# Kernel tuning notes

Hardware: AMD Instinct MI355X
Metric: run time of the kernel (lower is better)

Reference implementation:

```python
import jax, jax.numpy as jnp
import numpy as np

D, H, L, E, K, FF, VIS, NC, NT = 1024, 8, 4, 4, 2, 2048, 1536, 4, 4
HD = D // H


def layer_norm(x, g, b, eps=1e-5):
    m = x.mean(-1, keepdims=True)
    v = ((x - m) ** 2).mean(-1, keepdims=True)
    return (x - m) / jnp.sqrt(v + eps) * g + b


def sinusoidal_pos(seq_len):
    pos = jnp.arange(seq_len, dtype=jnp.float32)[:, None]
    div = jnp.exp(jnp.arange(0, D, 2, dtype=jnp.float32) * (-jnp.log(10000.0) / D))
    pe = jnp.zeros((seq_len, D), dtype=jnp.float32)
    pe = pe.at[:, 0::2].set(jnp.sin(pos * div))
    pe = pe.at[:, 1::2].set(jnp.cos(pos * div))
    return pe


def mha(x, wi, bi, wo, bo):
    # wi: [D, 3D] (pre-transposed), wo: [D, D]
    B, S, _ = x.shape
    qkv = x @ wi + bi
    q, k, v = jnp.split(qkv, 3, axis=-1)
    split = lambda t: t.reshape(B, S, H, HD).transpose(0, 2, 1, 3)
    q, k, v = split(q), split(k), split(v)
    scores = jnp.einsum('bhqd,bhkd->bhqk', q, k) / jnp.sqrt(jnp.float32(HD))
    a = jax.nn.softmax(scores, axis=-1)
    o = jnp.einsum('bhqk,bhkd->bhqd', a, v).transpose(0, 2, 1, 3).reshape(B, S, D)
    return o @ wo + bo


def moe(x_flat, rw, rb, w1, b1, w2, b2):
    # x_flat: [N, D]; rw: [D, E]; w1: [E, D, FF]; w2: [E, FF, D]
    logits = x_flat @ rw + rb                      # [N, E]
    topv, topi = jax.lax.top_k(logits, K)          # [N, K]
    probs = jax.nn.softmax(topv, axis=-1)          # softmax over the top-k logits
    onehot = jax.nn.one_hot(topi, E, dtype=x_flat.dtype)      # [N, K, E]
    combine = jnp.einsum('nk,nke->ne', probs, onehot)         # [N, E]
    h = jax.nn.relu(jnp.einsum('nd,edf->enf', x_flat, w1) + b1[:, None, :])  # [E, N, FF]
    o = jnp.einsum('enf,efd->end', h, w2) + b2[:, None, :]                   # [E, N, D]
    return jnp.einsum('ne,end->nd', combine, o)


def setup_inputs() -> dict:
    key = jax.random.key(0)
    ks = iter(jax.random.split(key, 32))
    s = 0.02
    n = lambda shape: jax.random.normal(next(ks), shape, dtype=jnp.float32) * s
    inp = {
        'vis_feat': jax.random.normal(next(ks), (64, 128, VIS), dtype=jnp.float32),
        'proj_w': n((VIS, D)), 'proj_b': jnp.zeros((D,), jnp.float32),
        'in_proj_w': n((L, D, 3 * D)), 'in_proj_b': jnp.zeros((L, 3 * D), jnp.float32),
        'out_proj_w': n((L, D, D)), 'out_proj_b': jnp.zeros((L, D), jnp.float32),
        'ln1_g': jnp.ones((L, D), jnp.float32), 'ln1_b': jnp.zeros((L, D), jnp.float32),
        'ln2_g': jnp.ones((L, D), jnp.float32), 'ln2_b': jnp.zeros((L, D), jnp.float32),
        'router_w': n((L, D, E)), 'router_b': jnp.zeros((L, E), jnp.float32),
        'ew1': n((L, E, D, FF)), 'eb1': jnp.zeros((L, E, FF), jnp.float32),
        'ew2': n((L, E, FF, D)), 'eb2': jnp.zeros((L, E, D), jnp.float32),
        'attn_w': n((D, 1)), 'attn_b': jnp.zeros((1,), jnp.float32),
        'heads_w': n((NT, D, NC)), 'heads_b': jnp.zeros((NT, NC), jnp.float32),
    }
    return inp


def reference(vis_feat, proj_w, proj_b, in_proj_w, in_proj_b, out_proj_w, out_proj_b,
              ln1_g, ln1_b, ln2_g, ln2_b, router_w, router_b, ew1, eb1, ew2, eb2,
              attn_w, attn_b, heads_w, heads_b):
    B, S, _ = vis_feat.shape
    x = vis_feat @ proj_w + proj_b            # projection to d_model=1024
    x = x + sinusoidal_pos(S)[None]           # positional encoding
    for l in range(L):                         # 4 MoE transformer layers
        x = layer_norm(x + mha(x, in_proj_w[l], in_proj_b[l], out_proj_w[l], out_proj_b[l]),
                       ln1_g[l], ln1_b[l])
        moe_out = moe(x.reshape(B * S, D), router_w[l], router_b[l],
                      ew1[l], eb1[l], ew2[l], eb2[l]).reshape(B, S, D)
        x = layer_norm(x + moe_out, ln2_g[l], ln2_b[l])
    # attention pooling over time, then 4 task heads
    scores = jax.nn.softmax(x @ attn_w + attn_b, axis=1)   # [B, S, 1]
    pooled = jnp.sum(scores * x, axis=1)                   # [B, D]
    logits = jnp.einsum('bd,tdc->tbc', pooled, heads_w) + heads_b[:, None, :]  # [4, B, 4]
    return logits
```

## Files before the change

### kernel.cpp

```cpp
#include <hip/hip_runtime.h>
#include <hip/hip_bf16.h>

typedef unsigned short u16;
typedef unsigned int u32;
using short8 = __attribute__((ext_vector_type(8))) short;
using f32x4  = __attribute__((ext_vector_type(4))) float;

__device__ __forceinline__ u16 f2bu(float f) {
  u32 u = __builtin_bit_cast(u32, f);
  u32 r = u + 0x7fffu + ((u >> 16) & 1u);
  return (u16)(r >> 16);
}
__device__ __forceinline__ float bu2f(u16 u) {
  u32 x = ((u32)u) << 16;
  return __builtin_bit_cast(float, x);
}
__device__ __forceinline__ float waveRedSum(float v) {
  #pragma unroll
  for (int off = 32; off > 0; off >>= 1) v += __shfl_xor(v, off, 64);
  return v;
}
__device__ __forceinline__ void gload16(const void* g, void* l) {
  __builtin_amdgcn_global_load_lds((const __attribute__((address_space(1))) u32*)g,
                                   (__attribute__((address_space(3))) u32*)l, 16, 0, 0);
}

template<int MODE>
__global__ __launch_bounds__(256) void gemm_bt(
    const u16* __restrict__ A, const u16* __restrict__ Bt, const float* __restrict__ bias,
    float* __restrict__ Cf, u16* __restrict__ Cb, u16* __restrict__ M0, u16* __restrict__ M1,
    const int* __restrict__ tok, const float* __restrict__ prob, const int* __restrict__ slot,
    const int* __restrict__ poff, const int* __restrict__ cnts,
    int N, int K)
{
  const int gx = gridDim.x;
  const int nwg = gx * gridDim.y;
  int lid = blockIdx.y * gx + blockIdx.x;
  lid = (lid & 7) * (nwg >> 3) + (lid >> 3);
  const int brow = (lid / gx) << 7, bcol = (lid % gx) << 7;

  int e = 0, rowEnd = 0;
  const u16* Bw = Bt;
  const float* bw = bias;
  if constexpr (MODE >= 2) {
    if (brow >= poff[4]) return;
    #pragma unroll
    for (int q = 1; q < 4; ++q) if (brow >= poff[q]) e = q;
    rowEnd = poff[e] + cnts[e];
    Bw = Bt + (size_t)e * N * K;
    bw = bias + e * N;
  }

  __shared__ __align__(16) u16 As[128 * 32];
  __shared__ __align__(16) u16 Bs[128 * 32];
  const int tid = threadIdx.x;
  const int wave = tid >> 6, lane = tid & 63;
  const int wr = wave >> 1, wc = wave & 1;
  const int r = lane & 15, kg = lane >> 4;

  f32x4 acc[4][4];
  #pragma unroll
  for (int m = 0; m < 4; ++m)
    #pragma unroll
    for (int n = 0; n < 4; ++n) acc[m][n] = f32x4{0.f, 0.f, 0.f, 0.f};

  const int c0 = (wave << 6) + lane;
  const int row0 = c0 >> 2, col0 = (c0 & 3) << 3;
  const int c1 = 256 + c0;
  const int row1 = c1 >> 2, col1 = (c1 & 3) << 3;

  size_t ar0, ar1;
  if constexpr (MODE == 2) {
    const int g0 = brow + row0, g1 = brow + row1;
    ar0 = (size_t)tok[(g0 < rowEnd) ? g0 : poff[e]];
    ar1 = (size_t)tok[(g1 < rowEnd) ? g1 : poff[e]];
  } else {
    ar0 = (size_t)(brow + row0);
    ar1 = (size_t)(brow + row1);
  }
  const u16* Bb = Bw + (size_t)bcol * K;

  for (int k0 = 0; k0 < K; k0 += 32) {
    __syncthreads();
    gload16(A + ar0 * K + k0 + col0, &As[(wave << 6) * 8]);
    gload16(Bb + (size_t)row0 * K + k0 + col0, &Bs[(wave << 6) * 8]);
    gload16(A + ar1 * K + k0 + col1, &As[(256 + (wave << 6)) * 8]);
    gload16(Bb + (size_t)row1 * K + k0 + col1, &Bs[(256 + (wave << 6)) * 8]);
    __syncthreads();
    short8 a[4], b[4];
    #pragma unroll
    for (int m = 0; m < 4; ++m)
      a[m] = *(const short8*)&As[((wr << 6) + (m << 4) + r) * 32 + (kg << 3)];
    #pragma unroll
    for (int n = 0; n < 4; ++n)
      b[n] = *(const short8*)&Bs[((wc << 6) + (n << 4) + r) * 32 + (kg << 3)];
    #pragma unroll
    for (int m = 0; m < 4; ++m)
      #pragma unroll
      for (int n = 0; n < 4; ++n)
        acc[m][n] = __builtin_amdgcn_mfma_f32_16x16x32_bf16(a[m], b[n], acc[m][n], 0, 0, 0);
  }

  if constexpr (MODE == 3) {
    #pragma unroll
    for (int m = 0; m < 4; ++m) {
      #pragma unroll
      for (int i4 = 0; i4 < 4; ++i4) {
        const int row = brow + (wr << 6) + (m << 4) + (kg << 2) + i4;
        if (row < rowEnd) {
          const int t = tok[row];
          const float pp = prob[row];
          u16* dst = slot[row] ? M1 : M0;
          #pragma unroll
          for (int n = 0; n < 4; ++n) {
            const int col = bcol + (wc << 6) + (n << 4) + r;
            dst[(size_t)t * N + col] = f2bu((acc[m][n][i4] + bw[col]) * pp);
          }
        }
      }
    }
  } else {
    #pragma unroll
    for (int m = 0; m < 4; ++m) {
      #pragma unroll
      for (int n = 0; n < 4; ++n) {
        const int col = bcol + (wc << 6) + (n << 4) + r;
        const float bv = bw[col];
        #pragma unroll
        for (int i4 = 0; i4 < 4; ++i4) {
          const int row = brow + (wr << 6) + (m << 4) + (kg << 2) + i4;
          const float v = acc[m][n][i4] + bv;
          const size_t off = (size_t)row * N + col;
          if constexpr (MODE == 0) Cf[off] = v;
          else if constexpr (MODE == 1) Cb[off] = f2bu(v);
          else Cb[off] = f2bu(fmaxf(v, 0.f));
        }
      }
    }
  }
}

__device__ __forceinline__ void tconv_tile(const float* __restrict__ s, u16* __restrict__ d,
                                           int K, int N, int n0, int k0)
{
  __shared__ float t[32][33];
  const int x = threadIdx.x, y = threadIdx.y;
  #pragma unroll
  for (int j = 0; j < 4; ++j) t[y + 8 * j][x] = s[(size_t)(k0 + y + 8 * j) * N + n0 + x];
  __syncthreads();
  #pragma unroll
  for (int j = 0; j < 4; ++j) d[(size_t)(n0 + y + 8 * j) * K + k0 + x] = f2bu(t[x][y + 8 * j]);
}

__global__ __launch_bounds__(256) void tconv_kernel(const float* __restrict__ src, u16* __restrict__ dst,
                                                    int K, int N)
{
  tconv_tile(src, dst, K, N, blockIdx.x << 5, blockIdx.y << 5);
}

__global__ __launch_bounds__(256) void tconv4_kernel(
    const float* __restrict__ wqkv_s, const float* __restrict__ wout_s,
    const float* __restrict__ we1_s, const float* __restrict__ we2_s,
    u16* __restrict__ wqkv_d, u16* __restrict__ wout_d,
    u16* __restrict__ we1_d, u16* __restrict__ we2_d)
{
  const int bid = blockIdx.x;
  if (bid < 3072) {
    tconv_tile(wqkv_s, wqkv_d, 1024, 3072, (bid % 96) << 5, (bid / 96) << 5);
  } else if (bid < 4096) {
    const int b2 = bid - 3072;
    tconv_tile(wout_s, wout_d, 1024, 1024, (b2 % 32) << 5, (b2 / 32) << 5);
  } else if (bid < 12288) {
    const int b2 = bid - 4096;
    const int ee = b2 >> 11, rr = b2 & 2047;
    tconv_tile(we1_s + (size_t)ee * 2048 * 1024, we1_d + (size_t)ee * 2048 * 1024,
               1024, 2048, (rr % 64) << 5, (rr / 64) << 5);
  } else {
    const int b2 = bid - 12288;
    const int ee = b2 >> 11, rr = b2 & 2047;
    tconv_tile(we2_s + (size_t)ee * 1024 * 2048, we2_d + (size_t)ee * 1024 * 2048,
               2048, 1024, (rr % 32) << 5, (rr / 32) << 5);
  }
}

__global__ __launch_bounds__(256) void conv_kernel(const float* __restrict__ in, u16* __restrict__ out)
{
  const size_t i = ((size_t)blockIdx.x * 256 + threadIdx.x) * 4;
  float4 v = *(const float4*)(in + i);
  *(ushort4*)(out + i) = make_ushort4(f2bu(v.x), f2bu(v.y), f2bu(v.z), f2bu(v.w));
}

__global__ __launch_bounds__(256) void pe_kernel(float* __restrict__ X, u16* __restrict__ Xb)
{
  const int idx = blockIdx.x * 256 + threadIdx.x;
  const int d = idx & 1023;
  const int s = (idx >> 10) & 127;
  const float de = (float)(d & ~1);
  const float ang = (float)s * expf(de * (-9.210340371976184f / 1024.f));
  const float pe = (d & 1) ? cosf(ang) : sinf(ang);
  const float v = X[idx] + pe;
  X[idx] = v;
  Xb[idx] = f2bu(v);
}

__global__ __launch_bounds__(256) void ln_kernel(const float* __restrict__ Xi, const u16* __restrict__ R,
    const float* __restrict__ g, const float* __restrict__ be,
    const float* __restrict__ rw, const float* __restrict__ rb,
    float* __restrict__ Xo, u16* __restrict__ Xbo,
    int* __restrict__ choice, float* __restrict__ prob2)
{
  const int token = blockIdx.x;
  const size_t base = (size_t)token << 10;
  const int tid = threadIdx.x;
  float vals[4]; float s = 0.f, s2 = 0.f;
  #pragma unroll
  for (int j = 0; j < 4; ++j) {
    const int d = tid + (j << 8);
    const float v = Xi[base + d] + bu2f(R[base + d]);
    vals[j] = v; s += v; s2 += v * v;
  }
  s = waveRedSum(s); s2 = waveRedSum(s2);
  __shared__ float rs[4], rs2[4];
  __shared__ float rl[4][4];
  const int wave = tid >> 6, lane = tid & 63;
  if (lane == 0) { rs[wave] = s; rs2[wave] = s2; }
  __syncthreads();
  s = rs[0] + rs[1] + rs[2] + rs[3];
  s2 = rs2[0] + rs2[1] + rs2[2] + rs2[3];
  const float mean = s * (1.f / 1024.f);
  const float var = s2 * (1.f / 1024.f) - mean * mean;
  const float inv = rsqrtf(var + 1e-5f);
  float l0 = 0.f, l1 = 0.f, l2 = 0.f, l3 = 0.f;
  #pragma unroll
  for (int j = 0; j < 4; ++j) {
    const int d = tid + (j << 8);
    const float y = (vals[j] - mean) * inv * g[d] + be[d];
    Xo[base + d] = y;
    Xbo[base + d] = f2bu(y);
    const float4 w = *(const float4*)(rw + ((size_t)d << 2));
    l0 += y * w.x; l1 += y * w.y; l2 += y * w.z; l3 += y * w.w;
  }
  l0 = waveRedSum(l0); l1 = waveRedSum(l1); l2 = waveRedSum(l2); l3 = waveRedSum(l3);
  if (lane == 0) { rl[wave][0] = l0; rl[wave][1] = l1; rl[wave][2] = l2; rl[wave][3] = l3; }
  __syncthreads();
  if (tid == 0) {
    float v[4];
    #pragma unroll
    for (int q = 0; q < 4; ++q)
      v[q] = rl[0][q] + rl[1][q] + rl[2][q] + rl[3][q] + rb[q];
    int i1 = 0;
    for (int q = 1; q < 4; ++q) if (v[q] > v[i1]) i1 = q;
    int i2 = (i1 == 0) ? 1 : 0;
    for (int q = 0; q < 4; ++q) if (q != i1 && v[q] > v[i2]) i2 = q;
    const float p2 = __expf(v[i2] - v[i1]);
    const float is = 1.f / (1.f + p2);
    choice[token] = i1 | (i2 << 8);
    prob2[token * 2]     = is;
    prob2[token * 2 + 1] = p2 * is;
  }
}

__global__ __launch_bounds__(256) void ln2_kernel(const float* __restrict__ Xi,
    const u16* __restrict__ R0, const u16* __restrict__ R1,
    const float* __restrict__ g, const float* __restrict__ be,
    float* __restrict__ Xo, u16* __restrict__ Xbo,
    const float* __restrict__ aw, const float* __restrict__ ab, float* __restrict__ S)
{
  const int token = blockIdx.x;
  const size_t base = (size_t)token << 10;
  const int tid = threadIdx.x;
  float vals[4]; float s = 0.f, s2 = 0.f;
  #pragma unroll
  for (int j = 0; j < 4; ++j) {
    const int d = tid + (j << 8);
    const float v = Xi[base + d] + (bu2f(R0[base + d]) + bu2f(R1[base + d]));
    vals[j] = v; s += v; s2 += v * v;
  }
  s = waveRedSum(s); s2 = waveRedSum(s2);
  __shared__ float rs[4], rs2[4];
  __shared__ float rsc[4];
  const int wave = tid >> 6, lane = tid & 63;
  if (lane == 0) { rs[wave] = s; rs2[wave] = s2; }
  __syncthreads();
  s = rs[0] + rs[1] + rs[2] + rs[3];
  s2 = rs2[0] + rs2[1] + rs2[2] + rs2[3];
  const float mean = s * (1.f / 1024.f);
  const float var = s2 * (1.f / 1024.f) - mean * mean;
  const float inv = rsqrtf(var + 1e-5f);
  float sc = 0.f;
  #pragma unroll
  for (int j = 0; j < 4; ++j) {
    const int d = tid + (j << 8);
    const float y = (vals[j] - mean) * inv * g[d] + be[d];
    Xo[base + d] = y;
    Xbo[base + d] = f2bu(y);
    if (aw) sc += y * aw[d];
  }
  if (aw) {
    sc = waveRedSum(sc);
    if (lane == 0) rsc[wave] = sc;
    __syncthreads();
    if (tid == 0) S[token] = rsc[0] + rsc[1] + rsc[2] + rsc[3] + ab[0];
  }
}

#define LDW 136
__global__ __launch_bounds__(256) void attn_mfma_kernel(const u16* __restrict__ QKVb, u16* __restrict__ ATTb)
{
  __shared__ __align__(16) u16 Kb[128 * LDW];
  __shared__ __align__(16) u16 Vt[128 * LDW];
  u16* Pb = Kb;
  const int b = blockIdx.x >> 3, h = blockIdx.x & 7;
  const int tid = threadIdx.x;
  const int wave = tid >> 6, lane = tid & 63;
  const int r = lane & 15, kg = lane >> 4;
  const u16* base = QKVb + (size_t)b * 128 * 3072 + h * 128;

  for (int i = tid; i < 128 * 16; i += 256) {
    const int row = i >> 4, c8 = (i & 15) << 3;
    *(short8*)&Kb[row * LDW + c8] = *(const short8*)(base + (size_t)row * 3072 + 1024 + c8);
  }
  for (int i = tid; i < 128 * 128; i += 256) {
    const int d = i & 127, key = i >> 7;
    Vt[d * LDW + key] = base[(size_t)key * 3072 + 2048 + d];
  }

  short8 a[2][4];
  #pragma unroll
  for (int m = 0; m < 2; ++m) {
    const int row = wave * 32 + m * 16 + r;
    const u16* qp = base + (size_t)row * 3072;
    #pragma unroll
    for (int ks = 0; ks < 4; ++ks)
      a[m][ks] = *(const short8*)(qp + ks * 32 + kg * 8);
  }
  __syncthreads();

  f32x4 acc[2][8];
  #pragma unroll
  for (int m = 0; m < 2; ++m)
    #pragma unroll
    for (int n = 0; n < 8; ++n) acc[m][n] = f32x4{0.f, 0.f, 0.f, 0.f};
  #pragma unroll
  for (int n = 0; n < 8; ++n) {
    #pragma unroll
    for (int ks = 0; ks < 4; ++ks) {
      short8 bf = *(const short8*)&Kb[(n * 16 + r) * LDW + ks * 32 + kg * 8];
      #pragma unroll
      for (int m = 0; m < 2; ++m)
        acc[m][n] = __builtin_amdgcn_mfma_f32_16x16x32_bf16(a[m][ks], bf, acc[m][n], 0, 0, 0);
    }
  }
  __syncthreads();

  const float sc = 0.08838834764831845f;
  #pragma unroll
  for (int m = 0; m < 2; ++m) {
    #pragma unroll
    for (int i = 0; i < 4; ++i) {
      float mx = -1e30f;
      #pragma unroll
      for (int n = 0; n < 8; ++n) mx = fmaxf(mx, acc[m][n][i]);
      #pragma unroll
      for (int msk = 1; msk < 16; msk <<= 1) mx = fmaxf(mx, __shfl_xor(mx, msk, 64));
      float s = 0.f;
      #pragma unroll
      for (int n = 0; n < 8; ++n) { float pv = __expf((acc[m][n][i] - mx) * sc); acc[m][n][i] = pv; s += pv; }
      #pragma unroll
      for (int msk = 1; msk < 16; msk <<= 1) s += __shfl_xor(s, msk, 64);
      const float inv = 1.f / s;
      #pragma unroll
      for (int n = 0; n < 8; ++n) {
        const int prow = wave * 32 + m * 16 + kg * 4 + i;
        Pb[prow * LDW + n * 16 + r] = f2bu(acc[m][n][i] * inv);
      }
    }
  }

  f32x4 oacc[2][8];
  #pragma unroll
  for (int m = 0; m < 2; ++m)
    #pragma unroll
    for (int n = 0; n < 8; ++n) oacc[m][n] = f32x4{0.f, 0.f, 0.f, 0.f};
  #pragma unroll
  for (int ks = 0; ks < 4; ++ks) {
    short8 pa[2];
    #pragma unroll
    for (int m = 0; m < 2; ++m)
      pa[m] = *(const short8*)&Pb[(wave * 32 + m * 16 + r) * LDW + ks * 32 + kg * 8];
    #pragma unroll
    for (int n = 0; n < 8; ++n) {
      short8 vb = *(const short8*)&Vt[(n * 16 + r) * LDW + ks * 32 + kg * 8];
      #pragma unroll
      for (int m = 0; m < 2; ++m)
        oacc[m][n] = __builtin_amdgcn_mfma_f32_16x16x32_bf16(pa[m], vb, oacc[m][n], 0, 0, 0);
    }
  }

  u16* op = ATTb + ((size_t)b * 128) * 1024 + h * 128;
  #pragma unroll
  for (int m = 0; m < 2; ++m) {
    #pragma unroll
    for (int n = 0; n < 8; ++n) {
      #pragma unroll
      for (int i = 0; i < 4; ++i) {
        const int row = wave * 32 + m * 16 + kg * 4 + i;
        op[(size_t)row * 1024 + n * 16 + r] = f2bu(oacc[m][n][i]);
      }
    }
  }
}
#undef LDW

__global__ __launch_bounds__(256) void build_lists_kernel(
    const int* __restrict__ choice, const float* __restrict__ prob2,
    int* __restrict__ cnt, int* __restrict__ poff,
    int* __restrict__ tok, float* __restrict__ prob, int* __restrict__ slot)
{
  const int tid = threadIdx.x;
  const int e = tid >> 6, lane = tid & 63;
  const int t0 = lane << 7;
  int mycount = 0;
  for (int j = 0; j < 128; ++j) {
    const int c = choice[t0 + j];
    mycount += (((c & 255) == e) || ((c >> 8) == e)) ? 1 : 0;
  }
  int incl = mycount;
  #pragma unroll
  for (int off = 1; off < 64; off <<= 1) {
    const int t = __shfl_up(incl, off, 64);
    if (lane >= off) incl += t;
  }
  __shared__ int totals[4];
  if (lane == 63) totals[e] = incl;
  __syncthreads();
  int base = 0;
  #pragma unroll
  for (int q = 0; q < 4; ++q)
    if (q < e) base += (totals[q] + 255) & ~255;
  int pos = base + incl - mycount;
  for (int j = 0; j < 128; ++j) {
    const int token = t0 + j;
    const int c = choice[token];
    const int m = ((c & 255) == e) ? 1 : (((c >> 8) == e) ? 2 : 0);
    if (m) {
      tok[pos] = token;
      prob[pos] = prob2[token * 2 + (m - 1)];
      slot[pos] = m - 1;
      ++pos;
    }
  }
  if (lane == 0) {
    cnt[e] = totals[e];
    poff[e] = base;
    if (e == 3) poff[4] = base + ((totals[3] + 255) & ~255);
  }
}

__global__ __launch_bounds__(256) void pool_kernel(const float* __restrict__ X, const float* __restrict__ S,
                                                   float* __restrict__ P)
{
  const int b = blockIdx.x;
  const int tid = threadIdx.x;
  __shared__ float p[128];
  if (tid < 128) p[tid] = S[b * 128 + tid];
  __syncthreads();
  float mx = -1e30f;
  for (int t = 0; t < 128; ++t) mx = fmaxf(mx, p[t]);
  float sum = 0.f;
  for (int t = 0; t < 128; ++t) sum += __expf(p[t] - mx);
  const float inv = 1.f / sum;
  __syncthreads();
  if (tid < 128) p[tid] = __expf(p[tid] - mx) * inv;
  __syncthreads();
  float acc[4] = {0.f, 0.f, 0.f, 0.f};
  for (int t = 0; t < 128; ++t) {
    const float pt = p[t];
    const float* xp = X + ((size_t)(b * 128 + t) << 10) + tid;
    #pragma unroll
    for (int j = 0; j < 4; ++j) acc[j] += pt * xp[j << 8];
  }
  #pragma unroll
  for (int j = 0; j < 4; ++j) P[((size_t)b << 10) + tid + (j << 8)] = acc[j];
}

__global__ __launch_bounds__(256) void heads_kernel(const float* __restrict__ P, const float* __restrict__ hw,
    const float* __restrict__ hb, float* __restrict__ out)
{
  const int idx = blockIdx.x * 4 + (threadIdx.x >> 6);
  const int lane = threadIdx.x & 63;
  const int t = idx >> 8, b = (idx >> 2) & 63, c = idx & 3;
  const float* pp = P + ((size_t)b << 10);
  const float* wp = hw + (size_t)t * 4096 + c;
  float s = 0.f;
  #pragma unroll
  for (int j = 0; j < 16; ++j) { const int k = lane + (j << 6); s += pp[k] * wp[(size_t)k << 2]; }
  s = waveRedSum(s);
  if (lane == 0) out[idx] = s + hb[t * 4 + c];
}

extern "C" void kernel_launch(void* const* d_in, const int* in_sizes, int n_in,
                              void* d_out, int out_size, void* d_ws, size_t ws_size,
                              hipStream_t stream)
{
  (void)in_sizes; (void)n_in; (void)out_size; (void)ws_size;
  const float* vis        = (const float*)d_in[0];
  const float* proj_w     = (const float*)d_in[1];
  const float* proj_b     = (const float*)d_in[2];
  const float* in_proj_w  = (const float*)d_in[3];
  const float* in_proj_b  = (const float*)d_in[4];
  const float* out_proj_w = (const float*)d_in[5];
  const float* out_proj_b = (const float*)d_in[6];
  const float* ln1_g      = (const float*)d_in[7];
  const float* ln1_b      = (const float*)d_in[8];
  const float* ln2_g      = (const float*)d_in[9];
  const float* ln2_b      = (const float*)d_in[10];
  const float* router_w   = (const float*)d_in[11];
  const float* router_b   = (const float*)d_in[12];
  const float* ew1        = (const float*)d_in[13];
  const float* eb1        = (const float*)d_in[14];
  const float* ew2        = (const float*)d_in[15];
  const float* eb2        = (const float*)d_in[16];
  const float* attn_w     = (const float*)d_in[17];
  const float* attn_b     = (const float*)d_in[18];
  const float* heads_w    = (const float*)d_in[19];
  const float* heads_b    = (const float*)d_in[20];
  float* out = (float*)d_out;

  char* p = (char*)d_ws;
  auto take = [&](size_t bytes) -> char* {
    char* q = p; p += (bytes + 255) & ~(size_t)255; return q;
  };
  float* X    = (float*)take(8192ULL * 1024 * 4);
  u16*   Xb   = (u16*)  take(8192ULL * 1024 * 2);
  char*  QKVr = take(104857600ULL);
  u16*   ATTb = (u16*)  take(8192ULL * 1024 * 2);
  int*   CNT  = (int*)  take(4 * 4);
  int*   POFF = (int*)  take(5 * 4);
  int*   CHOICE = (int*)take(8192ULL * 4);
  float* PROB2  = (float*)take(8192ULL * 2 * 4);
  int*   TOK  = (int*)  take(17408ULL * 4);
  float* PROB = (float*)take(17408ULL * 4);
  int*   SLOT = (int*)  take(17408ULL * 4);
  float* S    = (float*)take(8192ULL * 4);
  float* POOL = (float*)take(64ULL * 1024 * 4);
  u16*   Wqkv = (u16*)  take(3072ULL * 1024 * 2);
  u16*   Wout = (u16*)  take(1024ULL * 1024 * 2);
  u16*   We1  = (u16*)  take(4ULL * 2048 * 1024 * 2);
  u16*   We2  = (u16*)  take(4ULL * 1024 * 2048 * 2);
  u16*   QKVb  = (u16*)QKVr;
  u16*   O16   = (u16*)QKVr;
  u16*   H     = (u16*)QKVr;
  u16*   MOE0b = (u16*)(QKVr + 71303168);
  u16*   MOE1b = (u16*)(QKVr + 71303168 + 16777216);
  u16*   Wproj = We1;
  u16*   VISb  = (u16*)QKVr;

  const dim3 tb(32, 8);
  #define GARGS Cf_, Cb_, MOE0b, MOE1b, TOK, PROB, SLOT, POFF, CNT

  tconv_kernel<<<dim3(1024 / 32, 1536 / 32), tb, 0, stream>>>(proj_w, Wproj, 1536, 1024);
  conv_kernel<<<(8192 * 1536 / 4) / 256, 256, 0, stream>>>(vis, VISb);
  {
    float* Cf_ = X; u16* Cb_ = nullptr;
    gemm_bt<0><<<dim3(8, 64), 256, 0, stream>>>(VISb, Wproj, proj_b, GARGS, 1024, 1536);
  }
  pe_kernel<<<8192 * 1024 / 256, 256, 0, stream>>>(X, Xb);

  for (int l = 0; l < 4; ++l) {
    tconv4_kernel<<<20480, tb, 0, stream>>>(
        in_proj_w + (size_t)l * 1024 * 3072, out_proj_w + (size_t)l * 1024 * 1024,
        ew1 + (size_t)l * 4 * 1024 * 2048, ew2 + (size_t)l * 4 * 2048 * 1024,
        Wqkv, Wout, We1, We2);

    {
      float* Cf_ = nullptr; u16* Cb_ = QKVb;
      gemm_bt<1><<<dim3(24, 64), 256, 0, stream>>>(Xb, Wqkv, in_proj_b + l * 3072, GARGS, 3072, 1024);
    }
    attn_mfma_kernel<<<512, 256, 0, stream>>>(QKVb, ATTb);
    {
      float* Cf_ = nullptr; u16* Cb_ = O16;
      gemm_bt<1><<<dim3(8, 64), 256, 0, stream>>>(ATTb, Wout, out_proj_b + l * 1024, GARGS, 1024, 1024);
    }
    ln_kernel<<<8192, 256, 0, stream>>>(X, O16, ln1_g + l * 1024, ln1_b + l * 1024,
                                        router_w + (size_t)l * 4096, router_b + l * 4,
                                        X, Xb, CHOICE, PROB2);
    build_lists_kernel<<<1, 256, 0, stream>>>(CHOICE, PROB2, CNT, POFF, TOK, PROB, SLOT);
    {
      float* Cf_ = nullptr; u16* Cb_ = H;
      gemm_bt<2><<<dim3(16, 136), 256, 0, stream>>>(Xb, We1, eb1 + (size_t)l * 4 * 2048, GARGS, 2048, 1024);
    }
    {
      float* Cf_ = nullptr; u16* Cb_ = nullptr;
      gemm_bt<3><<<dim3(8, 136), 256, 0, stream>>>(H, We2, eb2 + (size_t)l * 4 * 1024, GARGS, 1024, 2048);
    }
    ln2_kernel<<<8192, 256, 0, stream>>>(X, MOE0b, MOE1b, ln2_g + l * 1024, ln2_b + l * 1024,
                                         X, Xb, (l == 3) ? attn_w : nullptr, attn_b, S);
  }

  pool_kernel<<<64, 256, 0, stream>>>(X, S, POOL);
  heads_kernel<<<256, 256, 0, stream>>>(POOL, heads_w, heads_b, out);
  #undef GARGS
}
```

Before: 1.962 ms.

## Replace 128x128 GEMM with 256x256 double-buffered swizzled 8-wave kernel

Swaps the single-buffered 128x128x32 bf16 GEMM for a 512-thread kernel computing 256x256 tiles with a K step of 64. Tiles are staged through double-buffered, XOR-swizzled LDS using direct global-to-LDS loads. The main loop interleaves the prefetch loads with four MFMA quarters, separated by explicit sched barriers, waitcnt and setprio. The aim is more data reuse per loaded byte, fewer LDS bank conflicts, and overlap of global loads with matrix math. The trade-offs are lower occupancy (one large block per CU, 128 KB of LDS) and 256-row tiles in the MoE grouped GEMMs, which assumes the expert row offsets line up with the larger tile.

```diff
diff --git a/kernel.cpp b/kernel.cpp
--- a/kernel.cpp
+++ b/kernel.cpp
@@ -25,8 +25,12 @@
                                    (__attribute__((address_space(3))) u32*)l, 16, 0, 0);
 }
 
+#define SB() __builtin_amdgcn_sched_barrier(0)
+#define BARR() do { SB(); __builtin_amdgcn_s_barrier(); SB(); } while (0)
+#define VMC2() do { SB(); asm volatile("s_waitcnt vmcnt(2)" ::: "memory"); SB(); } while (0)
+
 template<int MODE>
-__global__ __launch_bounds__(256) void gemm_bt(
+__global__ __launch_bounds__(512, 1) void gemm8(
     const u16* __restrict__ A, const u16* __restrict__ Bt, const float* __restrict__ bias,
     float* __restrict__ Cf, u16* __restrict__ Cb, u16* __restrict__ M0, u16* __restrict__ M1,
     const int* __restrict__ tok, const float* __restrict__ prob, const int* __restrict__ slot,
@@ -37,7 +41,7 @@
   const int nwg = gx * gridDim.y;
   int lid = blockIdx.y * gx + blockIdx.x;
   lid = (lid & 7) * (nwg >> 3) + (lid >> 3);
-  const int brow = (lid / gx) << 7, bcol = (lid % gx) << 7;
+  const int brow = (lid / gx) << 8, bcol = (lid % gx) << 8;
 
   int e = 0, rowEnd = 0;
   const u16* Bw = Bt;
@@ -51,62 +55,98 @@
     bw = bias + e * N;
   }
 
-  __shared__ __align__(16) u16 As[128 * 32];
-  __shared__ __align__(16) u16 Bs[128 * 32];
+  __shared__ __align__(16) u16 As[32768];
+  __shared__ __align__(16) u16 Bs[32768];
+
   const int tid = threadIdx.x;
   const int wave = tid >> 6, lane = tid & 63;
-  const int wr = wave >> 1, wc = wave & 1;
+  const int wr = wave >> 2, wc = wave & 3;
   const int r = lane & 15, kg = lane >> 4;
 
-  f32x4 acc[4][4];
-  #pragma unroll
-  for (int m = 0; m < 4; ++m)
+  const int srow = tid >> 3;
+  const int sc8 = (tid & 7) ^ (srow & 7);
+
+  int tokA[2][2];
+  if constexpr (MODE == 2) {
+    #pragma unroll
+    for (int h = 0; h < 2; ++h)
+      #pragma unroll
+      for (int j = 0; j < 2; ++j) {
+        const int g = brow + h * 128 + srow + j * 64;
+        tokA[h][j] = tok[(g < rowEnd) ? g : poff[e]];
+      }
+  }
+
+#define STA(c, kt, h) do { \
+  _Pragma("unroll") for (int j_ = 0; j_ < 2; ++j_) { \
+    size_t gr_; \
+    if constexpr (MODE == 2) gr_ = (size_t)tokA[h][j_]; \
+    else gr_ = (size_t)(brow + (h) * 128 + srow + j_ * 64); \
+    gload16(A + gr_ * K + ((kt) << 6) + (sc8 << 3), \
+            &As[((c) << 14) + ((h) << 13) + (j_ << 12) + (tid << 3)]); \
+  } } while (0)
+
+#define STB(c, kt, h) do { \
+  _Pragma("unroll") for (int j_ = 0; j_ < 2; ++j_) { \
+    const size_t gr_ = (size_t)(bcol + (h) * 128 + srow + j_ * 64); \
+    gload16(Bw + gr_ * K + ((kt) << 6) + (sc8 << 3), \
+            &Bs[((c) << 14) + ((h) << 13) + (j_ << 12) + (tid << 3)]); \
+  } } while (0)
+
+  short8 afr[4], bfr[4];
+  f32x4 acc[8][4];
+  #pragma unroll
+  for (int m = 0; m < 8; ++m)
     #pragma unroll
     for (int n = 0; n < 4; ++n) acc[m][n] = f32x4{0.f, 0.f, 0.f, 0.f};
 
-  const int c0 = (wave << 6) + lane;
-  const int row0 = c0 >> 2, col0 = (c0 & 3) << 3;
-  const int c1 = 256 + c0;
-  const int row1 = c1 >> 2, col1 = (c1 & 3) << 3;
-
-  size_t ar0, ar1;
-  if constexpr (MODE == 2) {
-    const int g0 = brow + row0, g1 = brow + row1;
-    ar0 = (size_t)tok[(g0 < rowEnd) ? g0 : poff[e]];
-    ar1 = (size_t)tok[(g1 < rowEnd) ? g1 : poff[e]];
-  } else {
-    ar0 = (size_t)(brow + row0);
-    ar1 = (size_t)(brow + row1);
-  }
-  const u16* Bb = Bw + (size_t)bcol * K;
-
-  for (int k0 = 0; k0 < K; k0 += 32) {
-    __syncthreads();
-    gload16(A + ar0 * K + k0 + col0, &As[(wave << 6) * 8]);
-    gload16(Bb + (size_t)row0 * K + k0 + col0, &Bs[(wave << 6) * 8]);
-    gload16(A + ar1 * K + k0 + col1, &As[(256 + (wave << 6)) * 8]);
-    gload16(Bb + (size_t)row1 * K + k0 + col1, &Bs[(256 + (wave << 6)) * 8]);
-    __syncthreads();
-    short8 a[4], b[4];
-    #pragma unroll
-    for (int m = 0; m < 4; ++m)
-      a[m] = *(const short8*)&As[((wr << 6) + (m << 4) + r) * 32 + (kg << 3)];
-    #pragma unroll
-    for (int n = 0; n < 4; ++n)
-      b[n] = *(const short8*)&Bs[((wc << 6) + (n << 4) + r) * 32 + (kg << 3)];
-    #pragma unroll
-    for (int m = 0; m < 4; ++m)
-      #pragma unroll
-      for (int n = 0; n < 4; ++n)
-        acc[m][n] = __builtin_amdgcn_mfma_f32_16x16x32_bf16(a[m], b[n], acc[m][n], 0, 0, 0);
+#define LDA(c, MQ, KS) { _Pragma("unroll") for (int mm = 0; mm < 4; ++mm) { \
+    const int Rl = (MQ) * 64 + mm * 16 + r; \
+    const int c8 = (KS) * 4 + kg; \
+    afr[mm] = *(const short8*)&As[((c) << 14) + (wr << 13) + Rl * 64 + ((c8 ^ (Rl & 7)) << 3)]; } }
+#define LDB(c, KS) { _Pragma("unroll") for (int nn = 0; nn < 4; ++nn) { \
+    const int colL = wc * 64 + nn * 16 + r; \
+    const int c8 = (KS) * 4 + kg; \
+    const int Rl = colL & 127; \
+    bfr[nn] = *(const short8*)&Bs[((c) << 14) + ((colL >> 7) << 13) + Rl * 64 + ((c8 ^ (Rl & 7)) << 3)]; } }
+#define MFMAQ(MQ) do { __builtin_amdgcn_s_setprio(1); \
+  _Pragma("unroll") for (int nn = 0; nn < 4; ++nn) \
+  _Pragma("unroll") for (int mm = 0; mm < 4; ++mm) \
+    acc[(MQ) * 4 + mm][nn] = __builtin_amdgcn_mfma_f32_16x16x32_bf16(afr[mm], bfr[nn], acc[(MQ) * 4 + mm][nn], 0, 0, 0); \
+  __builtin_amdgcn_s_setprio(0); } while (0)
+
+  const int NT = K >> 6;
+  STB(0, 0, 0); STB(0, 0, 1); STA(0, 0, 0); STA(0, 0, 1);
+  STB(1, 1, 0);
+  VMC2();
+  BARR();
+
+  for (int t = 0; t < NT; ++t) {
+    const int cb = t & 1, nb = cb ^ 1;
+    int t1 = t + 1; if (t1 >= NT) t1 -= NT;
+    int t2 = t + 2; if (t2 >= NT) t2 -= NT;
+    LDA(cb, 0, 0); LDB(cb, 0);
+    STB(nb, t1, 1);
+    BARR(); MFMAQ(0); BARR();
+    LDA(cb, 1, 0);
+    STA(nb, t1, 0);
+    BARR(); MFMAQ(1); BARR();
+    LDA(cb, 0, 1); LDB(cb, 1);
+    STA(nb, t1, 1);
+    BARR(); MFMAQ(0); BARR();
+    LDA(cb, 1, 1);
+    STB(cb, t2, 0);
+    VMC2();
+    BARR();
+    MFMAQ(1); BARR();
   }
 
   if constexpr (MODE == 3) {
     #pragma unroll
-    for (int m = 0; m < 4; ++m) {
+    for (int m = 0; m < 8; ++m) {
       #pragma unroll
       for (int i4 = 0; i4 < 4; ++i4) {
-        const int row = brow + (wr << 6) + (m << 4) + (kg << 2) + i4;
+        const int row = brow + (wr << 7) + (m << 4) + (kg << 2) + i4;
         if (row < rowEnd) {
           const int t = tok[row];
           const float pp = prob[row];
@@ -121,14 +161,14 @@
     }
   } else {
     #pragma unroll
-    for (int m = 0; m < 4; ++m) {
+    for (int m = 0; m < 8; ++m) {
       #pragma unroll
       for (int n = 0; n < 4; ++n) {
         const int col = bcol + (wc << 6) + (n << 4) + r;
         const float bv = bw[col];
         #pragma unroll
         for (int i4 = 0; i4 < 4; ++i4) {
-          const int row = brow + (wr << 6) + (m << 4) + (kg << 2) + i4;
+          const int row = brow + (wr << 7) + (m << 4) + (kg << 2) + i4;
           const float v = acc[m][n][i4] + bv;
           const size_t off = (size_t)row * N + col;
           if constexpr (MODE == 0) Cf[off] = v;
@@ -138,6 +178,11 @@
       }
     }
   }
+#undef STA
+#undef STB
+#undef LDA
+#undef LDB
+#undef MFMAQ
 }
 
 __device__ __forceinline__ void tconv_tile(const float* __restrict__ s, u16* __restrict__ d,
@@ -563,7 +608,7 @@
   conv_kernel<<<(8192 * 1536 / 4) / 256, 256, 0, stream>>>(vis, VISb);
   {
     float* Cf_ = X; u16* Cb_ = nullptr;
-    gemm_bt<0><<<dim3(8, 64), 256, 0, stream>>>(VISb, Wproj, proj_b, GARGS, 1024, 1536);
+    gemm8<0><<<dim3(4, 32), 512, 0, stream>>>(VISb, Wproj, proj_b, GARGS, 1024, 1536);
   }
   pe_kernel<<<8192 * 1024 / 256, 256, 0, stream>>>(X, Xb);
 
@@ -575,12 +620,12 @@
 
     {
       float* Cf_ = nullptr; u16* Cb_ = QKVb;
-      gemm_bt<1><<<dim3(24, 64), 256, 0, stream>>>(Xb, Wqkv, in_proj_b + l * 3072, GARGS, 3072, 1024);
+      gemm8<1><<<dim3(12, 32), 512, 0, stream>>>(Xb, Wqkv, in_proj_b + l * 3072, GARGS, 3072, 1024);
     }
     attn_mfma_kernel<<<512, 256, 0, stream>>>(QKVb, ATTb);
     {
       float* Cf_ = nullptr; u16* Cb_ = O16;
-      gemm_bt<1><<<dim3(8, 64), 256, 0, stream>>>(ATTb, Wout, out_proj_b + l * 1024, GARGS, 1024, 1024);
+      gemm8<1><<<dim3(4, 32), 512, 0, stream>>>(ATTb, Wout, out_proj_b + l * 1024, GARGS, 1024, 1024);
     }
     ln_kernel<<<8192, 256, 0, stream>>>(X, O16, ln1_g + l * 1024, ln1_b + l * 1024,
                                         router_w + (size_t)l * 4096, router_b + l * 4,
@@ -588,11 +633,11 @@
     build_lists_kernel<<<1, 256, 0, stream>>>(CHOICE, PROB2, CNT, POFF, TOK, PROB, SLOT);
     {
       float* Cf_ = nullptr; u16* Cb_ = H;
-      gemm_bt<2><<<dim3(16, 136), 256, 0, stream>>>(Xb, We1, eb1 + (size_t)l * 4 * 2048, GARGS, 2048, 1024);
+      gemm8<2><<<dim3(8, 68), 512, 0, stream>>>(Xb, We1, eb1 + (size_t)l * 4 * 2048, GARGS, 2048, 1024);
     }
     {
       float* Cf_ = nullptr; u16* Cb_ = nullptr;
-      gemm_bt<3><<<dim3(8, 136), 256, 0, stream>>>(H, We2, eb2 + (size_t)l * 4 * 1024, GARGS, 1024, 2048);
+      gemm8<3><<<dim3(4, 68), 512, 0, stream>>>(H, We2, eb2 + (size_t)l * 4 * 1024, GARGS, 1024, 2048);
     }
     ln2_kernel<<<8192, 256, 0, stream>>>(X, MOE0b, MOE1b, ln2_g + l * 1024, ln2_b + l * 1024,
                                          X, Xb, (l == 3) ? attn_w : nullptr, attn_b, S);
```

New measurement: 2.113 ms. 7.7% more time.

## Double GEMM K-tile to 64 and XOR-swizzle LDS to avoid bank conflicts

Applied to the files above, without the earlier changes.

The bf16 MFMA GEMM now stages a 128x64 K-slice of A and B per iteration instead of 128x32. That halves the number of barrier pairs per K and gives two MFMA sub-steps per load. The LDS layout is XOR-swizzled on 16-byte chunks by row, so fragment reads from rows with the 128-byte stride avoid bank conflicts. Global source pointers, including the gathered token rows in MODE 2, are precomputed once outside the K loop. LDS use doubles to 32 KB per block, which may reduce occupancy, and K must be a multiple of 64.

```diff
diff --git a/kernel.cpp b/kernel.cpp
--- a/kernel.cpp
+++ b/kernel.cpp
@@ -51,8 +51,8 @@
     bw = bias + e * N;
   }
 
-  __shared__ __align__(16) u16 As[128 * 32];
-  __shared__ __align__(16) u16 Bs[128 * 32];
+  __shared__ __align__(16) u16 As[128 * 64];
+  __shared__ __align__(16) u16 Bs[128 * 64];
   const int tid = threadIdx.x;
   const int wave = tid >> 6, lane = tid & 63;
   const int wr = wave >> 1, wc = wave & 1;
@@ -64,41 +64,51 @@
     #pragma unroll
     for (int n = 0; n < 4; ++n) acc[m][n] = f32x4{0.f, 0.f, 0.f, 0.f};
 
-  const int c0 = (wave << 6) + lane;
-  const int row0 = c0 >> 2, col0 = (c0 & 3) << 3;
-  const int c1 = 256 + c0;
-  const int row1 = c1 >> 2, col1 = (c1 & 3) << 3;
-
-  size_t ar0, ar1;
-  if constexpr (MODE == 2) {
-    const int g0 = brow + row0, g1 = brow + row1;
-    ar0 = (size_t)tok[(g0 < rowEnd) ? g0 : poff[e]];
-    ar1 = (size_t)tok[(g1 < rowEnd) ? g1 : poff[e]];
-  } else {
-    ar0 = (size_t)(brow + row0);
-    ar1 = (size_t)(brow + row1);
-  }
+  const u16* aSrc[4];
+  const u16* bSrc[4];
   const u16* Bb = Bw + (size_t)bcol * K;
-
-  for (int k0 = 0; k0 < K; k0 += 32) {
+  #pragma unroll
+  for (int q = 0; q < 4; ++q) {
+    const int cid = (q << 8) + (wave << 6) + lane;
+    const int row = cid >> 3, c = cid & 7;
+    const int scol = (c ^ (row & 7)) << 3;
+    size_t ar;
+    if constexpr (MODE == 2) {
+      const int g = brow + row;
+      ar = (size_t)tok[(g < rowEnd) ? g : poff[e]];
+    } else {
+      ar = (size_t)(brow + row);
+    }
+    aSrc[q] = A + ar * K + scol;
+    bSrc[q] = Bb + (size_t)row * K + scol;
+  }
+  const int swz0 = (kg ^ (r & 7)) << 3;
+  const int swz1 = ((4 + kg) ^ (r & 7)) << 3;
+
+  for (int k0 = 0; k0 < K; k0 += 64) {
     __syncthreads();
-    gload16(A + ar0 * K + k0 + col0, &As[(wave << 6) * 8]);
-    gload16(Bb + (size_t)row0 * K + k0 + col0, &Bs[(wave << 6) * 8]);
-    gload16(A + ar1 * K + k0 + col1, &As[(256 + (wave << 6)) * 8]);
-    gload16(Bb + (size_t)row1 * K + k0 + col1, &Bs[(256 + (wave << 6)) * 8]);
+    #pragma unroll
+    for (int q = 0; q < 4; ++q) {
+      gload16(aSrc[q] + k0, &As[(((q << 8) + (wave << 6))) << 3]);
+      gload16(bSrc[q] + k0, &Bs[(((q << 8) + (wave << 6))) << 3]);
+    }
     __syncthreads();
-    short8 a[4], b[4];
-    #pragma unroll
-    for (int m = 0; m < 4; ++m)
-      a[m] = *(const short8*)&As[((wr << 6) + (m << 4) + r) * 32 + (kg << 3)];
-    #pragma unroll
-    for (int n = 0; n < 4; ++n)
-      b[n] = *(const short8*)&Bs[((wc << 6) + (n << 4) + r) * 32 + (kg << 3)];
-    #pragma unroll
-    for (int m = 0; m < 4; ++m)
+    #pragma unroll
+    for (int ks = 0; ks < 2; ++ks) {
+      const int swz = ks ? swz1 : swz0;
+      short8 a[4], b[4];
+      #pragma unroll
+      for (int m = 0; m < 4; ++m)
+        a[m] = *(const short8*)&As[(((wr << 6) + (m << 4) + r) << 6) + swz];
       #pragma unroll
       for (int n = 0; n < 4; ++n)
-        acc[m][n] = __builtin_amdgcn_mfma_f32_16x16x32_bf16(a[m], b[n], acc[m][n], 0, 0, 0);
+        b[n] = *(const short8*)&Bs[(((wc << 6) + (n << 4) + r) << 6) + swz];
+      #pragma unroll
+      for (int m = 0; m < 4; ++m)
+        #pragma unroll
+        for (int n = 0; n < 4; ++n)
+          acc[m][n] = __builtin_amdgcn_mfma_f32_16x16x32_bf16(a[m], b[n], acc[m][n], 0, 0, 0);
+    }
   }
 
   if constexpr (MODE == 3) {
```

After: 1.844 ms. 1.06x faster.
